# Kernel tuning notes

Hardware: AMD Instinct MI355X
Metric: run time of the kernel (lower is better)

## Reference

```python
import jax, jax.numpy as jnp
import numpy as np

N_HEAD = 16
HEAD_DIM = 64
HIDDEN = 1024
ROPE_BASE = 10000.0


def _rope_tables(L, d):
    # inv_freq over even indices, emb = concat([freqs, freqs]) -> [L, d]
    inv_freq = 1.0 / (ROPE_BASE ** (jnp.arange(0, d, 2, dtype=jnp.float32) / d))
    freqs = jnp.arange(L, dtype=jnp.float32)[:, None] * inv_freq[None, :]  # [L, d/2]
    emb = jnp.concatenate([freqs, freqs], axis=-1)  # [L, d]
    return jnp.cos(emb), jnp.sin(emb)


def _rotate_half(t):
    d2 = t.shape[-1] // 2
    return jnp.concatenate([-t[..., d2:], t[..., :d2]], axis=-1)


def setup_inputs() -> dict:
    key = jax.random.key(0)
    ks = jax.random.split(key, 5)
    B, L = 1, 4096
    x = jax.random.normal(ks[0], (B, L, HIDDEN), dtype=jnp.float32)
    sc = 1.0 / np.sqrt(HIDDEN)
    wq = jax.random.normal(ks[1], (HIDDEN, HIDDEN), dtype=jnp.float32) * sc
    wk = jax.random.normal(ks[2], (HIDDEN, HIDDEN), dtype=jnp.float32) * sc
    wv = jax.random.normal(ks[3], (HIDDEN, HIDDEN), dtype=jnp.float32) * sc
    wo = jax.random.normal(ks[4], (HIDDEN, HIDDEN), dtype=jnp.float32) * sc
    return {"x": x, "wq": wq, "wk": wk, "wv": wv, "wo": wo}


def reference(x, wq, wk, wv, wo):
    B, L, D = x.shape
    H, Hd = N_HEAD, HEAD_DIM
    # projections (torch Linear: y = x @ W^T), split heads -> [B, H, L, Hd]
    q = jnp.einsum('bld,ed->ble', x, wq).reshape(B, L, H, Hd).transpose(0, 2, 1, 3)
    k = jnp.einsum('bld,ed->ble', x, wk).reshape(B, L, H, Hd).transpose(0, 2, 1, 3)
    v = jnp.einsum('bld,ed->ble', x, wv).reshape(B, L, H, Hd).transpose(0, 2, 1, 3)
    cos, sin = _rope_tables(L, Hd)  # [L, Hd]
    q = q * cos[None, None] + _rotate_half(q) * sin[None, None]
    k = k * cos[None, None] + _rotate_half(k) * sin[None, None]
    # causal SDPA, scale = 1/sqrt(head_dim)
    scores = jnp.einsum('bhqd,bhkd->bhqk', q, k) / jnp.sqrt(jnp.float32(Hd))
    causal = jnp.tril(jnp.ones((L, L), dtype=bool))
    scores = jnp.where(causal[None, None], scores, jnp.finfo(scores.dtype).min)
    attn = jax.nn.softmax(scores, axis=-1)
    out = jnp.einsum('bhqk,bhkd->bhqd', attn, v)  # [B, H, L, Hd]
    out = out.transpose(0, 2, 1, 3).reshape(B, L, D)
    return jnp.einsum('bld,ed->ble', out, wo)
```

## Files before the change

### kernel.cpp

```cpp
#include <hip/hip_runtime.h>
#include <math.h>
#include <type_traits>

constexpr int DM = 1024;
constexpr int NH = 16;
constexpr int HD = 64;
constexpr int LDQ = 3072;

typedef __attribute__((ext_vector_type(8))) short bf16x8;
typedef __attribute__((ext_vector_type(4))) float f32x4;

__device__ __forceinline__ unsigned short f2bf(float f) {
    union { float f; unsigned u; } v; v.f = f;
    unsigned r = v.u + 0x7FFFu + ((v.u >> 16) & 1u);
    return (unsigned short)(r >> 16);
}
__device__ __forceinline__ float bf2f(unsigned short h) {
    union { unsigned u; float f; } v; v.u = ((unsigned)h) << 16;
    return v.f;
}
__device__ __forceinline__ void gload16(const unsigned short* g, unsigned short* lds) {
    __builtin_amdgcn_global_load_lds(
        (const __attribute__((address_space(1))) unsigned int*)g,
        (__attribute__((address_space(3))) unsigned int*)lds, 16, 0, 0);
}
__device__ __forceinline__ unsigned cvt_pk_bf16(float lo, float hi) {
    unsigned r;
    asm("v_cvt_pk_bf16_f32 %0, %1, %2" : "=v"(r) : "v"(lo), "v"(hi));
    return r;
}
#define MFMA_BF16(a, b, c) __builtin_amdgcn_mfma_f32_16x16x32_bf16(a, b, c, 0, 0, 0)

__device__ __forceinline__ bf16x8 pack_swap(const f32x4& s0, const f32x4& s1) {
    unsigned c00 = cvt_pk_bf16(s0[0], s0[1]);
    unsigned c01 = cvt_pk_bf16(s0[2], s0[3]);
    unsigned c10 = cvt_pk_bf16(s1[0], s1[1]);
    unsigned c11 = cvt_pk_bf16(s1[2], s1[3]);
    asm("v_permlane32_swap_b32 %0, %1" : "+v"(c00), "+v"(c10));
    asm("v_permlane16_swap_b32 %0, %1" : "+v"(c00), "+v"(c10));
    asm("v_permlane32_swap_b32 %0, %1" : "+v"(c01), "+v"(c11));
    asm("v_permlane16_swap_b32 %0, %1" : "+v"(c01), "+v"(c11));
    union { unsigned u[4]; bf16x8 b; } r;
    r.u[0] = c00; r.u[1] = c01; r.u[2] = c10; r.u[3] = c11;
    return r.b;
}

__global__ __launch_bounds__(256)
void convert_bf16(const float* __restrict__ x, const float* __restrict__ wq,
                  const float* __restrict__ wk, const float* __restrict__ wv,
                  const float* __restrict__ wo, unsigned short* __restrict__ dst,
                  long long xElems) {
    const long long W = (long long)DM * DM;
    long long base = ((long long)blockIdx.x * 256 + threadIdx.x) * 8;
    const float* src; long long off;
    if (base < xElems) { src = x; off = base; }
    else {
        long long r = base - xElems;
        int wi = (int)(r / W); off = r - (long long)wi * W;
        src = wi == 0 ? wq : wi == 1 ? wk : wi == 2 ? wv : wo;
    }
    float4 a = *reinterpret_cast<const float4*>(src + off);
    float4 b = *reinterpret_cast<const float4*>(src + off + 4);
    uint4 o;
    o.x = (unsigned)f2bf(a.x) | ((unsigned)f2bf(a.y) << 16);
    o.y = (unsigned)f2bf(a.z) | ((unsigned)f2bf(a.w) << 16);
    o.z = (unsigned)f2bf(b.x) | ((unsigned)f2bf(b.y) << 16);
    o.w = (unsigned)f2bf(b.z) | ((unsigned)f2bf(b.w) << 16);
    *reinterpret_cast<uint4*>(dst + base) = o;
}

template <typename OT>
__global__ __launch_bounds__(256)
void gemm_bf16(const unsigned short* __restrict__ A, const unsigned short* __restrict__ B,
               OT* __restrict__ C, int M, int N, int K) {
    constexpr int BK = 32;
    __shared__ unsigned short As[128 * BK];
    __shared__ unsigned short Bs[128 * BK];
    const int t = threadIdx.x;
    const int w = t >> 6, l = t & 63;
    const int lg = l >> 4, ln = l & 15;
    const int bm = blockIdx.y * 128, bn = blockIdx.x * 128;
    const int wr = (w >> 1) * 64, wc = (w & 1) * 64;

    const int li0 = t, li1 = 256 + t;
    const int r0 = li0 >> 2, c0 = (li0 & 3) ^ ((r0 >> 1) & 3);
    const int r1 = li1 >> 2, c1 = (li1 & 3) ^ ((r1 >> 1) & 3);
    const unsigned short* gA0 = A + (size_t)(bm + r0) * K + c0 * 8;
    const unsigned short* gA1 = A + (size_t)(bm + r1) * K + c1 * 8;
    const unsigned short* gB0 = B + (size_t)(bn + r0) * K + c0 * 8;
    const unsigned short* gB1 = B + (size_t)(bn + r1) * K + c1 * 8;
    unsigned short* lA0 = As + (size_t)(w * 64) * 8;
    unsigned short* lA1 = As + (size_t)(256 + w * 64) * 8;
    unsigned short* lB0 = Bs + (size_t)(w * 64) * 8;
    unsigned short* lB1 = Bs + (size_t)(256 + w * 64) * 8;

    int aoff[4], boff[4];
#pragma unroll
    for (int m = 0; m < 4; ++m) { int R = wr + m * 16 + ln; aoff[m] = R * 64 + ((lg ^ ((R >> 1) & 3)) * 16); }
#pragma unroll
    for (int n = 0; n < 4; ++n) { int R = wc + n * 16 + ln; boff[n] = R * 64 + ((lg ^ ((R >> 1) & 3)) * 16); }

    const f32x4 z4 = {0.f, 0.f, 0.f, 0.f};
    f32x4 acc[4][4];
#pragma unroll
    for (int m = 0; m < 4; ++m)
#pragma unroll
        for (int n = 0; n < 4; ++n) acc[m][n] = z4;

    for (int k0 = 0; k0 < K; k0 += BK) {
        __syncthreads();
        gload16(gA0 + k0, lA0);
        gload16(gA1 + k0, lA1);
        gload16(gB0 + k0, lB0);
        gload16(gB1 + k0, lB1);
        __syncthreads();
        bf16x8 af[4], bfr[4];
#pragma unroll
        for (int m = 0; m < 4; ++m) af[m] = *(const bf16x8*)((const char*)As + aoff[m]);
#pragma unroll
        for (int n = 0; n < 4; ++n) bfr[n] = *(const bf16x8*)((const char*)Bs + boff[n]);
#pragma unroll
        for (int m = 0; m < 4; ++m)
#pragma unroll
            for (int n = 0; n < 4; ++n)
                acc[m][n] = MFMA_BF16(af[m], bfr[n], acc[m][n]);
    }

#pragma unroll
    for (int m = 0; m < 4; ++m)
#pragma unroll
        for (int n = 0; n < 4; ++n)
#pragma unroll
            for (int rg = 0; rg < 4; ++rg) {
                int row = bm + wr + m * 16 + lg * 4 + rg;
                int col = bn + wc + n * 16 + ln;
                if constexpr (std::is_same<OT, float>::value)
                    C[(size_t)row * N + col] = acc[m][n][rg];
                else
                    C[(size_t)row * N + col] = f2bf(acc[m][n][rg]);
            }
}

__global__ __launch_bounds__(512)
void rope_bf16(unsigned short* __restrict__ qkv) {
    constexpr float SCQ = 0.18033688011112042f;
    const int l = blockIdx.x;
    const int j = threadIdx.x & 31, h = threadIdx.x >> 5;
    const float inv = exp2f(-(float)j * (13.287712379549449f / 32.0f));
    const float ang = (float)l * inv;
    float s, c;
    sincosf(ang, &s, &c);
    const size_t base = (size_t)l * LDQ + h * HD + j;
    float a = bf2f(qkv[base]), b = bf2f(qkv[base + 32]);
    qkv[base]      = f2bf((a * c - b * s) * SCQ);
    qkv[base + 32] = f2bf((b * c + a * s) * SCQ);
    a = bf2f(qkv[base + DM]); b = bf2f(qkv[base + DM + 32]);
    qkv[base + DM]      = f2bf(a * c - b * s);
    qkv[base + DM + 32] = f2bf(b * c + a * s);
}

__global__ __launch_bounds__(256)
void transp_v(const unsigned short* __restrict__ qkv, unsigned short* __restrict__ vt,
              int L) {
    __shared__ unsigned LT[64][33];
    const int l0 = blockIdx.x * 64;
    const int h = blockIdx.y;
    const int t = threadIdx.x;
    const int jj = t >> 3;
    const int dc = t & 7;
    const unsigned short* vrow = qkv + 2 * DM + (size_t)(l0 + 2 * jj) * LDQ + h * HD + dc * 8;
    uint4 a = *reinterpret_cast<const uint4*>(vrow);
    uint4 b = *reinterpret_cast<const uint4*>(vrow + LDQ);
    const unsigned aw[4] = {a.x, a.y, a.z, a.w};
    const unsigned bw[4] = {b.x, b.y, b.z, b.w};
#pragma unroll
    for (int e = 0; e < 4; ++e) {
        LT[dc * 8 + e * 2][jj]     = __builtin_amdgcn_perm(bw[e], aw[e], 0x05040100u);
        LT[dc * 8 + e * 2 + 1][jj] = __builtin_amdgcn_perm(bw[e], aw[e], 0x07060302u);
    }
    __syncthreads();
#pragma unroll
    for (int it = 0; it < 2; ++it) {
        const int aidx = it * 256 + t;
        const int d = aidx >> 3, c = aidx & 7;
        uint4 o;
        o.x = LT[d][c * 4];     o.y = LT[d][c * 4 + 1];
        o.z = LT[d][c * 4 + 2]; o.w = LT[d][c * 4 + 3];
        *reinterpret_cast<uint4*>(vt + ((size_t)h * 64 + d) * L + l0 + c * 8) = o;
    }
}

__global__ __launch_bounds__(256)
void attn_mfma(const unsigned short* __restrict__ qkv,
               const unsigned short* __restrict__ vt,
               unsigned short* __restrict__ ob, int L) {
    __shared__ unsigned short Ks[2 * 4096];
    __shared__ unsigned short Vs[2 * 4096];
    __shared__ unsigned short Ps[32 * 72];

    const int bid = blockIdx.x;
    const int xcd = bid & 7, slot = bid >> 3;
    const int h = xcd + 8 * (slot & 1);
    const int nst = L / 64;
    const int st = nst - 1 - (slot >> 1);
    const int q0 = st * 64;
    const int t = threadIdx.x, w = t >> 6, l = t & 63;
    const int lg = l >> 4, ln = l & 15;

    const unsigned short* kga[2];
    const unsigned short* vga[2];
    int ldso[2];
#pragma unroll
    for (int i = 0; i < 2; ++i) {
        const int pc = t + 256 * i;
        const int r = pc >> 3, cc = (pc & 7) ^ (r & 7);
        kga[i] = qkv + DM + (size_t)r * LDQ + h * HD + cc * 8;
        vga[i] = vt + ((size_t)h * 64 + r) * L + cc * 8;
        ldso[i] = pc * 8;
    }

    int foff[4][2];
#pragma unroll
    for (int n = 0; n < 4; ++n)
#pragma unroll
        for (int ks = 0; ks < 2; ++ks) {
            const int R = n * 16 + ln;
            foff[n][ks] = R * 128 + (((ks * 4 + lg) ^ (R & 7)) * 16);
        }
    const int prow2 = ((w & 1) * 16 + ln) * 144;

    const f32x4 z4 = {0.f, 0.f, 0.f, 0.f};

    bf16x8 qf[2];
#pragma unroll
    for (int ks = 0; ks < 2; ++ks)
        qf[ks] = *reinterpret_cast<const bf16x8*>(
            qkv + (size_t)(q0 + w * 16 + ln) * LDQ + h * HD + ks * 32 + lg * 8);

    f32x4 oa[4];
#pragma unroll
    for (int dn = 0; dn < 4; ++dn) oa[dn] = z4;
    float m_i = -INFINITY, l_i = 0.f;

    const int ntk = st + 1;

#pragma unroll
    for (int i = 0; i < 2; ++i) gload16(kga[i], Ks + ldso[i]);
#pragma unroll
    for (int i = 0; i < 2; ++i) gload16(vga[i], Vs + ldso[i]);

    for (int kt = 0; kt < ntk; ++kt) {
        const int bsel = kt & 1;
        const int kv0 = kt * 64;
        const char* KsB = (const char*)(Ks + bsel * 4096);
        const char* VsB = (const char*)(Vs + bsel * 4096);

        asm volatile("s_waitcnt vmcnt(0)" ::: "memory");
        __builtin_amdgcn_sched_barrier(0);
        __builtin_amdgcn_s_barrier();
        __builtin_amdgcn_sched_barrier(0);
        if (kt + 1 < ntk) {
            const size_t kadv = (size_t)(kt + 1) * 64 * LDQ;
            const int vadv = (kt + 1) * 64;
            unsigned short* kd = Ks + (bsel ^ 1) * 4096;
            unsigned short* vd = Vs + (bsel ^ 1) * 4096;
#pragma unroll
            for (int i = 0; i < 2; ++i) gload16(kga[i] + kadv, kd + ldso[i]);
#pragma unroll
            for (int i = 0; i < 2; ++i) gload16(vga[i] + vadv, vd + ldso[i]);
        }

        bf16x8 kf[4][2];
#pragma unroll
        for (int n = 0; n < 4; ++n)
#pragma unroll
            for (int ks = 0; ks < 2; ++ks)
                kf[n][ks] = *reinterpret_cast<const bf16x8*>(KsB + foff[n][ks]);
        f32x4 s[4];
        __builtin_amdgcn_s_setprio(1);
#pragma unroll
        for (int n = 0; n < 4; ++n) {
            f32x4 acc = MFMA_BF16(kf[n][0], qf[0], z4);
            s[n] = MFMA_BF16(kf[n][1], qf[1], acc);
        }
        __builtin_amdgcn_s_setprio(0);

        if (kv0 + 63 > q0 + w * 16) {
            const int qq = q0 + w * 16 + ln;
#pragma unroll
            for (int n = 0; n < 4; ++n)
#pragma unroll
                for (int rg = 0; rg < 4; ++rg)
                    if (kv0 + n * 16 + lg * 4 + rg > qq) s[n][rg] = -INFINITY;
        }

        float mx = fmaxf(fmaxf(s[0][0], s[0][1]), fmaxf(s[0][2], s[0][3]));
#pragma unroll
        for (int n = 1; n < 4; ++n)
            mx = fmaxf(mx, fmaxf(fmaxf(s[n][0], s[n][1]),
                                 fmaxf(s[n][2], s[n][3])));
        mx = fmaxf(mx, __shfl_xor(mx, 16));
        mx = fmaxf(mx, __shfl_xor(mx, 32));
        if (__any(mx > m_i + 8.f)) {
            const float mn = fmaxf(m_i, mx);
            const float sc = exp2f(m_i - mn);
            m_i = mn;
            l_i *= sc;
#pragma unroll
            for (int dn = 0; dn < 4; ++dn) oa[dn] *= sc;
        }
        float ps = 0.f;
#pragma unroll
        for (int n = 0; n < 4; ++n)
#pragma unroll
            for (int rg = 0; rg < 4; ++rg) {
                const float pv = __builtin_amdgcn_exp2f(s[n][rg] - m_i);
                s[n][rg] = pv;
                ps += pv;
            }
        ps += __shfl_xor(ps, 16);
        ps += __shfl_xor(ps, 32);
        l_i += ps;

        bf16x8 pf0 = pack_swap(s[0], s[1]);
        bf16x8 pf1 = pack_swap(s[2], s[3]);

        bf16x8 vf[4][2];
#pragma unroll
        for (int dn = 0; dn < 4; ++dn)
#pragma unroll
            for (int ks = 0; ks < 2; ++ks)
                vf[dn][ks] = *reinterpret_cast<const bf16x8*>(VsB + foff[dn][ks]);
        __builtin_amdgcn_s_setprio(1);
#pragma unroll
        for (int dn = 0; dn < 4; ++dn) {
            oa[dn] = MFMA_BF16(vf[dn][0], pf0, oa[dn]);
            oa[dn] = MFMA_BF16(vf[dn][1], pf1, oa[dn]);
        }
        __builtin_amdgcn_s_setprio(0);
    }

    __syncthreads();
    {
        const float inv = 1.f / l_i;
        uint2 orow[4];
#pragma unroll
        for (int dn = 0; dn < 4; ++dn) {
            f32x4 o = oa[dn] * inv;
            orow[dn] = make_uint2(cvt_pk_bf16(o[0], o[1]), cvt_pk_bf16(o[2], o[3]));
        }
#pragma unroll
        for (int half = 0; half < 2; ++half) {
            if ((w >> 1) == half) {
#pragma unroll
                for (int dn = 0; dn < 4; ++dn)
                    *reinterpret_cast<uint2*>((char*)Ps + prow2 + dn * 32 + lg * 8) =
                        orow[dn];
            }
            __syncthreads();
            {
                const int r = t >> 3, c = (t & 7) * 8;
                const bf16x8 vv =
                    *reinterpret_cast<const bf16x8*>((const char*)Ps + r * 144 + c * 2);
                *reinterpret_cast<bf16x8*>(
                    ob + (size_t)(q0 + half * 32 + r) * DM + h * HD + c) = vv;
            }
            __syncthreads();
        }
    }
}

extern "C" void kernel_launch(void* const* d_in, const int* in_sizes, int n_in,
                              void* d_out, int out_size, void* d_ws, size_t ws_size,
                              hipStream_t stream) {
    const float* x  = (const float*)d_in[0];
    const float* wq = (const float*)d_in[1];
    const float* wk = (const float*)d_in[2];
    const float* wv = (const float*)d_in[3];
    const float* wo = (const float*)d_in[4];

    const int L = in_sizes[0] / DM;
    const size_t NE = (size_t)L * DM;
    const size_t W  = (size_t)DM * DM;

    unsigned short* xb   = (unsigned short*)d_ws;
    unsigned short* wqb  = xb + NE;
    unsigned short* wob  = wqb + 3 * W;
    unsigned short* qkvb = wob + W;
    unsigned short* ab   = qkvb + (size_t)L * LDQ;
    unsigned short* vtb  = (unsigned short*)d_out;

    const long long totalConv = (long long)(NE + 4 * W);
    convert_bf16<<<dim3((unsigned)(totalConv / 8 / 256)), dim3(256), 0, stream>>>(
        x, wq, wk, wv, wo, xb, (long long)NE);

    gemm_bf16<unsigned short><<<dim3(LDQ / 128, L / 128), dim3(256), 0, stream>>>(
        xb, wqb, qkvb, L, LDQ, DM);

    rope_bf16<<<dim3(L), dim3(512), 0, stream>>>(qkvb);

    transp_v<<<dim3(L / 64, NH), dim3(256), 0, stream>>>(qkvb, vtb, L);

    attn_mfma<<<dim3((L / 64) * NH), dim3(256), 0, stream>>>(qkvb, vtb, ab, L);

    gemm_bf16<float><<<dim3(DM / 128, L / 128), dim3(256), 0, stream>>>(
        ab, wob, (float*)d_out, L, DM, DM);
}
```

Before: 163.5 us.

## Split long causal query tiles across two KV halves and merge with a combine kernel

Result: no change. 161.2 us (-1.4%).

```diff
diff --git a/kernel.cpp b/kernel.cpp
--- a/kernel.cpp
+++ b/kernel.cpp
@@ -6,6 +6,8 @@
 constexpr int NH = 16;
 constexpr int HD = 64;
 constexpr int LDQ = 3072;
+constexpr int SPLIT_ST = 38;
+constexpr int PENT = 4224;
 
 typedef __attribute__((ext_vector_type(8))) short bf16x8;
 typedef __attribute__((ext_vector_type(4))) float f32x4;
@@ -193,17 +195,25 @@
 __global__ __launch_bounds__(256)
 void attn_mfma(const unsigned short* __restrict__ qkv,
                const unsigned short* __restrict__ vt,
-               unsigned short* __restrict__ ob, int L) {
+               unsigned short* __restrict__ ob,
+               float* __restrict__ pbuf, int L) {
     __shared__ unsigned short Ks[2 * 4096];
     __shared__ unsigned short Vs[2 * 4096];
     __shared__ unsigned short Ps[32 * 72];
 
     const int bid = blockIdx.x;
-    const int xcd = bid & 7, slot = bid >> 3;
-    const int h = xcd + 8 * (slot & 1);
-    const int nst = L / 64;
-    const int st = nst - 1 - (slot >> 1);
+    const int xcd = bid & 7, rest = bid >> 3;
+    const int h = xcd + 8 * (rest & 1);
+    const int j = rest >> 1;
+    int st, klo, khi;
+    if (j < 6)       { st = 37 - j;        klo = 0;  khi = st + 1; }
+    else if (j < 32) { st = 38 + (j - 6);  klo = 0;  khi = 32; }
+    else if (j < 58) { st = 63 - (j - 32); klo = 32; khi = st + 1; }
+    else             { st = 31 - (j - 58); klo = 0;  khi = st + 1; }
+    const bool partial = (j >= 6 && j < 58);
+    const int part = (j < 32) ? 0 : 1;
     const int q0 = st * 64;
+
     const int t = threadIdx.x, w = t >> 6, l = t & 63;
     const int lg = l >> 4, ln = l & 15;
 
@@ -242,15 +252,13 @@
     for (int dn = 0; dn < 4; ++dn) oa[dn] = z4;
     float m_i = -INFINITY, l_i = 0.f;
 
-    const int ntk = st + 1;
-
-#pragma unroll
-    for (int i = 0; i < 2; ++i) gload16(kga[i], Ks + ldso[i]);
-#pragma unroll
-    for (int i = 0; i < 2; ++i) gload16(vga[i], Vs + ldso[i]);
-
-    for (int kt = 0; kt < ntk; ++kt) {
-        const int bsel = kt & 1;
+#pragma unroll
+    for (int i = 0; i < 2; ++i) gload16(kga[i] + (size_t)klo * 64 * LDQ, Ks + ldso[i]);
+#pragma unroll
+    for (int i = 0; i < 2; ++i) gload16(vga[i] + klo * 64, Vs + ldso[i]);
+
+    for (int kt = klo; kt < khi; ++kt) {
+        const int bsel = (kt - klo) & 1;
         const int kv0 = kt * 64;
         const char* KsB = (const char*)(Ks + bsel * 4096);
         const char* VsB = (const char*)(Vs + bsel * 4096);
@@ -259,7 +267,7 @@
         __builtin_amdgcn_sched_barrier(0);
         __builtin_amdgcn_s_barrier();
         __builtin_amdgcn_sched_barrier(0);
-        if (kt + 1 < ntk) {
+        if (kt + 1 < khi) {
             const size_t kadv = (size_t)(kt + 1) * 64 * LDQ;
             const int vadv = (kt + 1) * 64;
             unsigned short* kd = Ks + (bsel ^ 1) * 4096;
@@ -341,7 +349,18 @@
     }
 
     __syncthreads();
-    {
+    if (partial) {
+        const int sidx = st - SPLIT_ST;
+        float* pb = pbuf + (size_t)((sidx * NH + h) * 2 + part) * PENT;
+        const int q = w * 16 + ln;
+#pragma unroll
+        for (int dn = 0; dn < 4; ++dn)
+            *reinterpret_cast<f32x4*>(pb + q * 64 + dn * 16 + lg * 4) = oa[dn];
+        if (lg == 0) {
+            pb[4096 + q] = m_i;
+            pb[4160 + q] = l_i;
+        }
+    } else {
         const float inv = 1.f / l_i;
         uint2 orow[4];
 #pragma unroll
@@ -370,6 +389,29 @@
     }
 }
 
+__global__ __launch_bounds__(256)
+void combine_split(const float* __restrict__ pbuf, unsigned short* __restrict__ ob) {
+    const int sidx = blockIdx.x, h = blockIdx.y;
+    const float* p0 = pbuf + (size_t)((sidx * NH + h) * 2 + 0) * PENT;
+    const float* p1 = pbuf + (size_t)((sidx * NH + h) * 2 + 1) * PENT;
+    const int t = threadIdx.x;
+    const int q = t >> 2, dg = (t & 3) * 16;
+    const float m1 = p0[4096 + q], l1 = p0[4160 + q];
+    const float m2 = p1[4096 + q], l2 = p1[4160 + q];
+    const float m = fmaxf(m1, m2);
+    const float w1 = exp2f(m1 - m), w2 = exp2f(m2 - m);
+    const float inv = 1.f / (w1 * l1 + w2 * l2);
+    const int q0 = (sidx + SPLIT_ST) * 64;
+#pragma unroll
+    for (int e = 0; e < 4; ++e) {
+        f32x4 a = *reinterpret_cast<const f32x4*>(p0 + q * 64 + dg + e * 4);
+        f32x4 b = *reinterpret_cast<const f32x4*>(p1 + q * 64 + dg + e * 4);
+        f32x4 o = (a * w1 + b * w2) * inv;
+        *reinterpret_cast<uint2*>(ob + (size_t)(q0 + q) * DM + h * HD + dg + e * 4) =
+            make_uint2(cvt_pk_bf16(o[0], o[1]), cvt_pk_bf16(o[2], o[3]));
+    }
+}
+
 extern "C" void kernel_launch(void* const* d_in, const int* in_sizes, int n_in,
                               void* d_out, int out_size, void* d_ws, size_t ws_size,
                               hipStream_t stream) {
@@ -389,6 +431,7 @@
     unsigned short* qkvb = wob + W;
     unsigned short* ab   = qkvb + (size_t)L * LDQ;
     unsigned short* vtb  = (unsigned short*)d_out;
+    float* pbuf = (float*)d_ws;
 
     const long long totalConv = (long long)(NE + 4 * W);
     convert_bf16<<<dim3((unsigned)(totalConv / 8 / 256)), dim3(256), 0, stream>>>(
@@ -401,7 +444,9 @@
 
     transp_v<<<dim3(L / 64, NH), dim3(256), 0, stream>>>(qkvb, vtb, L);
 
-    attn_mfma<<<dim3((L / 64) * NH), dim3(256), 0, stream>>>(qkvb, vtb, ab, L);
+    attn_mfma<<<dim3(90 * NH), dim3(256), 0, stream>>>(qkvb, vtb, ab, pbuf, L);
+
+    combine_split<<<dim3(64 - SPLIT_ST, NH), dim3(256), 0, stream>>>(pbuf, ab);
 
     gemm_bf16<float><<<dim3(DM / 128, L / 128), dim3(256), 0, stream>>>(
         ab, wob, (float*)d_out, L, DM, DM);
```
